# Optimization experiments

Hardware: AMD Instinct MI355X
Metric: run time of the kernel (lower is better)

## Reference

```python
import jax, jax.numpy as jnp
import numpy as np

B, J, L = 32, 16, 4096
MU_P = 0.15
MASK_ID = 103
VOCAB = 30522


def setup_inputs() -> dict:
    key = jax.random.key(0)
    k1, k2, k3 = jax.random.split(key, 3)
    input_ids = jax.random.randint(k1, (B, J, L), 0, VOCAB, dtype=jnp.int64 if jax.config.jax_enable_x64 else jnp.int32)
    # first half: nonnegative per-token weights; second half: shared-token ids (unused by the math)
    my_attention_mask = jax.random.uniform(k2, (B, J, 2 * L), dtype=jnp.float32)
    # uniform noise for Gumbel keys (weighted sampling w/o replacement)
    u = jax.random.uniform(k3, (B, J, L), dtype=jnp.float32, minval=1e-6, maxval=1.0)
    return {"input_ids": input_ids, "my_attention_mask": my_attention_mask, "u": u}


def reference(input_ids, my_attention_mask, u):
    # Split the mask: first half holds sampling weights (second half is unused).
    Lh = my_attention_mask.shape[-1] // 2
    w = my_attention_mask[..., :Lh]                       # [B, J, L]
    nz = w > 0                                            # valid positions
    cnt = nz.sum(axis=-1)                                 # [B, J] number of nonzero weights
    num_to_mask = jnp.floor(MU_P * cnt.astype(w.dtype)).astype(jnp.int32)  # int(mu_p * len)

    # Gumbel-key trick == weighted permutation without replacement over nonzero positions.
    g = -jnp.log(-jnp.log(u))
    scores = jnp.where(nz, jnp.log(jnp.maximum(w, 1e-30)) + g, -jnp.inf)
    # rank of each position in descending-score order
    rank = jnp.argsort(jnp.argsort(-scores, axis=-1), axis=-1)
    sel = (rank < num_to_mask[..., None]) & nz            # [B, J, L] positions to mask

    out_mask = sel.astype(w.dtype)
    out_ids = jnp.where(sel, jnp.asarray(MASK_ID, dtype=input_ids.dtype), input_ids)
    return out_ids, out_mask, -out_mask
```

## Files before the change

### kernel.cpp

```cpp
#include <hip/hip_runtime.h>

#define L_LEN 4096
#define NT 1024
#define ROWS 512
#define SLOP 96u
#define BCAP 256
#define NW (NT / 64)

__global__ __launch_bounds__(NT, 8) void AttentionEssentialReinforce_51238959841470_kernel(
    const int* __restrict__ ids,
    const float* __restrict__ amask,
    const float* __restrict__ uin,
    float* __restrict__ out,
    int n_per)
{
    __shared__ unsigned int hist[4096];
    __shared__ unsigned int h2[256];
    __shared__ unsigned int s_cntw[NW], s_orw[NW], s_nhiw[NW], s_wtot[NW];
    __shared__ unsigned long long bkey[BCAP];
    __shared__ int bidx[BCAP];
    __shared__ unsigned int s_remk, s_prefix, s_bn;

    const int row = blockIdx.x;
    const int tid = threadIdx.x;
    const int lane = tid & 63, wid = tid >> 6;
    const float* wrow = amask + (size_t)row * (2 * L_LEN);
    const float* urow = uin + (size_t)row * L_LEN;

    float4 a0 = reinterpret_cast<const float4*>(wrow)[tid];
    float4 b0 = reinterpret_cast<const float4*>(urow)[tid];
    unsigned odd = ((const unsigned*)ids)[2 * tid + 1];

    #pragma unroll
    for (int b = 0; b < 4096 / NT; ++b) hist[tid + b * NT] = 0u;
    if (tid < 256) h2[tid] = 0u;
    if (tid == 0) s_bn = 0u;

    float wv[4], uv[4];
    wv[0]=a0.x; wv[1]=a0.y; wv[2]=a0.z; wv[3]=a0.w;
    uv[0]=b0.x; uv[1]=b0.y; uv[2]=b0.z; uv[3]=b0.w;

    unsigned key[4];
    unsigned localnz = 0;
    #pragma unroll
    for (int e = 0; e < 4; ++e) {
        key[e] = 0u;
        if (wv[e] > 0.0f) {
            float t = -__logf(uv[e]);
            float r = __fdividef(fmaxf(wv[e], 1e-30f), t);
            key[e] = __float_as_uint(r);
            localnz++;
        }
    }
    {
        unsigned long long bal = __ballot(odd != 0u);
        unsigned v = localnz;
        #pragma unroll
        for (int off = 32; off > 0; off >>= 1) v += __shfl_down(v, off, 64);
        if (lane == 0) { s_cntw[wid] = v; s_orw[wid] = (bal != 0ull) ? 1u : 0u; }
    }
    __syncthreads();

    unsigned cnt = 0, orr = 0;
    #pragma unroll
    for (int w2 = 0; w2 < NW; ++w2) { cnt += s_cntw[w2]; orr |= s_orw[w2]; }
    const bool is64 = (orr == 0u);
    const int k = (int)floorf(0.15f * (float)cnt);

    int ida[4];
    if (!is64) {
        int4 t0 = reinterpret_cast<const int4*>(ids + (size_t)row * L_LEN)[tid];
        ida[0]=t0.x; ida[1]=t0.y; ida[2]=t0.z; ida[3]=t0.w;
    } else {
        const longlong2* idr = reinterpret_cast<const longlong2*>(
            (const long long*)ids + (size_t)row * L_LEN);
        longlong2 a = idr[2 * tid], b = idr[2 * tid + 1];
        ida[0]=(int)a.x; ida[1]=(int)a.y; ida[2]=(int)b.x; ida[3]=(int)b.y;
    }

    unsigned lo_thr = 0xFFFFFFFFu, hi_thr = 0xFFFFFFFFu;
    int need = 0;
    unsigned bn = 0;

    if (k > 0) {
        #pragma unroll
        for (int e = 0; e < 4; ++e) atomicAdd(&hist[key[e] >> 20], 1u);
        __syncthreads();
        {
            int b0i = 4095 - 4 * tid;
            unsigned c[4], lsum = 0;
            #pragma unroll
            for (int m = 0; m < 4; ++m) { c[m] = hist[b0i - m]; lsum += c[m]; }
            unsigned scan = lsum;
            #pragma unroll
            for (int off = 1; off < 64; off <<= 1) {
                unsigned o = __shfl_up(scan, (unsigned)off, 64);
                if (lane >= off) scan += o;
            }
            if (lane == 63) s_wtot[wid] = scan;
            __syncthreads();
            unsigned woff = 0;
            #pragma unroll
            for (int w2 = 0; w2 < NW; ++w2) woff += (w2 < wid) ? s_wtot[w2] : 0u;
            unsigned run = woff + (scan - lsum);
            unsigned remk = (unsigned)k;
            #pragma unroll
            for (int m = 0; m < 4; ++m) {
                if (run < remk && run + c[m] >= remk) {
                    s_prefix = (unsigned)(b0i - m);
                    s_remk = remk - run;
                }
                run += c[m];
            }
        }
        __syncthreads();
        unsigned prefix12 = s_prefix;
        unsigned remk = s_remk;

        #pragma unroll
        for (int e = 0; e < 4; ++e)
            if ((key[e] >> 20) == prefix12)
                atomicAdd(&h2[(key[e] >> 12) & 0xFFu], 1u);
        __syncthreads();
        if (tid < 64) {
            unsigned c[4], lsum = 0;
            #pragma unroll
            for (int m = 0; m < 4; ++m) { c[m] = h2[255 - 4 * tid - m]; lsum += c[m]; }
            unsigned scan = lsum;
            #pragma unroll
            for (int off = 1; off < 64; off <<= 1) {
                unsigned o = __shfl_up(scan, (unsigned)off, 64);
                if (tid >= off) scan += o;
            }
            unsigned run = scan - lsum;
            #pragma unroll
            for (int m = 0; m < 4; ++m) {
                if (run < remk && run + c[m] >= remk) {
                    s_prefix = (prefix12 << 8) | (unsigned)(255 - 4 * tid - m);
                }
                run += c[m];
            }
        }
        __syncthreads();
        const unsigned T20 = s_prefix;
        const unsigned B_lo = T20 << 12, B_hi = (T20 << 12) | 0xFFFu;

        lo_thr = (B_lo > SLOP) ? B_lo - SLOP : 1u;
        hi_thr = B_hi + SLOP;
        unsigned nhi = 0;
        #pragma unroll
        for (int e = 0; e < 4; ++e) {
            if (key[e] > hi_thr) {
                nhi++;
            } else if (key[e] >= lo_thr) {
                unsigned pos = atomicAdd(&s_bn, 1u);
                if (pos < BCAP) {
                    double t = -log((double)uv[e]);
                    double r = (double)fmaxf(wv[e], 1e-30f) / t;
                    bkey[pos] = (unsigned long long)__double_as_longlong(r);
                    bidx[pos] = 4 * tid + e;
                }
            }
        }
        {
            unsigned nv = nhi;
            #pragma unroll
            for (int off = 32; off > 0; off >>= 1) nv += __shfl_down(nv, off, 64);
            if (lane == 0) s_nhiw[wid] = nv;
        }
        __syncthreads();
        unsigned nhi_tot = 0;
        #pragma unroll
        for (int w2 = 0; w2 < NW; ++w2) nhi_tot += s_nhiw[w2];
        need = k - (int)nhi_tot;
        bn = s_bn; if (bn > BCAP) bn = BCAP;
    }

    const size_t obase = (size_t)row * L_LEN;
    float* o0 = out + obase;
    float* o1 = out + (size_t)n_per + obase;
    float* o2 = out + 2 * (size_t)n_per + obase;

    float f0[4], f1[4], f2[4];
    #pragma unroll
    for (int e = 0; e < 4; ++e) {
        bool sel;
        if (key[e] > hi_thr) {
            sel = true;
        } else if (key[e] < lo_thr) {
            sel = false;
        } else {
            double t = -log((double)uv[e]);
            double r = (double)fmaxf(wv[e], 1e-30f) / t;
            unsigned long long myk = (unsigned long long)__double_as_longlong(r);
            int myi = 4 * tid + e;
            int rnk = 0;
            for (unsigned j = 0; j < bn; ++j)
                rnk += (bkey[j] > myk) || (bkey[j] == myk && bidx[j] < myi);
            sel = (rnk < need);
        }
        f0[e] = sel ? 103.0f : (float)ida[e];
        f1[e] = sel ? 1.0f : 0.0f;
        f2[e] = sel ? -1.0f : -0.0f;
    }
    reinterpret_cast<float4*>(o0)[tid] = make_float4(f0[0], f0[1], f0[2], f0[3]);
    reinterpret_cast<float4*>(o1)[tid] = make_float4(f1[0], f1[1], f1[2], f1[3]);
    reinterpret_cast<float4*>(o2)[tid] = make_float4(f2[0], f2[1], f2[2], f2[3]);
}

extern "C" void kernel_launch(void* const* d_in, const int* in_sizes, int n_in,
                              void* d_out, int out_size, void* d_ws, size_t ws_size,
                              hipStream_t stream) {
    const int*   ids   = (const int*)d_in[0];
    const float* amask = (const float*)d_in[1];
    const float* uin   = (const float*)d_in[2];
    float* out = (float*)d_out;

    const int n_per = ROWS * L_LEN;

    AttentionEssentialReinforce_51238959841470_kernel<<<dim3(ROWS), dim3(NT), 0, stream>>>(
        ids, amask, uin, out, n_per);
}
```

Measured before the change: 86.56 us.

## Process two rows per block to hoist loads and overlap memory latency

Each 1024-thread block now handles two rows instead of one. All weight and noise loads for both rows, and the ids for both rows, are issued up front. The per-row selection phase is duplicated through a macro, with separate histogram and candidate buffers for each row. The goal is to hide global load latency behind the first row's compute, but the grid shrinks to 256 blocks on a GPU with many CUs, LDS per block doubles, and the launch-bounds occupancy hint drops.

```diff
diff --git a/kernel.cpp b/kernel.cpp
--- a/kernel.cpp
+++ b/kernel.cpp
@@ -7,205 +7,237 @@
 #define BCAP 256
 #define NW (NT / 64)
 
-__global__ __launch_bounds__(NT, 8) void AttentionEssentialReinforce_51238959841470_kernel(
+
+#define ROW_PHASE(R, AV, BV, IDA)                                                        \
+{                                                                                        \
+    float wv[4], uv[4];                                                                  \
+    wv[0]=AV.x; wv[1]=AV.y; wv[2]=AV.z; wv[3]=AV.w;                                      \
+    uv[0]=BV.x; uv[1]=BV.y; uv[2]=BV.z; uv[3]=BV.w;                                      \
+    unsigned key[4];                                                                     \
+    unsigned localnz = 0;                                                                \
+    _Pragma("unroll")                                                                    \
+    for (int e = 0; e < 4; ++e) {                                                        \
+        key[e] = 0u;                                 \
+        if (wv[e] > 0.0f) {                                                              \
+            float t = -__logf(uv[e]);                                                    \
+            float r = __fdividef(fmaxf(wv[e], 1e-30f), t);                               \
+            key[e] = __float_as_uint(r);                                                 \
+            localnz++;                                                                   \
+        }                                                                                \
+    }                                                                                    \
+    {                                                                                    \
+        unsigned v = localnz;                                                            \
+        _Pragma("unroll")                                                                \
+        for (int off = 32; off > 0; off >>= 1) v += __shfl_down(v, off, 64);             \
+        if (R == 0) {                                                                    \
+            unsigned long long bal = __ballot(odd != 0u);                                \
+            if (lane == 0) { s_cntw[R][wid] = v; s_orw[wid] = (bal != 0ull) ? 1u : 0u; } \
+        } else {                                                                         \
+            if (lane == 0) s_cntw[R][wid] = v;                                           \
+        }                                                                                \
+    }                                                                                    \
+    __syncthreads();                                     \
+    unsigned cnt = 0;                                                                    \
+    _Pragma("unroll")                                                                    \
+    for (int w2 = 0; w2 < NW; ++w2) cnt += s_cntw[R][w2];                                \
+    const int k = (int)floorf(0.15f * (float)cnt);      \
+    if (R == 0) {                                                                        \
+        unsigned orr = 0;                                                                \
+        _Pragma("unroll")                                                                \
+        for (int w2 = 0; w2 < NW; ++w2) orr |= s_orw[w2];                                \
+        is64 = (orr == 0u);                                                              \
+                  \
+                                         \
+        if (!is64) {                                                                     \
+            int4 t0 = reinterpret_cast<const int4*>(ids + (size_t)row0 * L_LEN)[tid];    \
+            ida0[0]=t0.x; ida0[1]=t0.y; ida0[2]=t0.z; ida0[3]=t0.w;                      \
+            int4 t1 = reinterpret_cast<const int4*>(ids + (size_t)(row0+1) * L_LEN)[tid];\
+            ida1[0]=t1.x; ida1[1]=t1.y; ida1[2]=t1.z; ida1[3]=t1.w;                      \
+        } else {                                                                         \
+            const long long* idp = (const long long*)ids;                                \
+            const longlong2* i0 = reinterpret_cast<const longlong2*>(                    \
+                idp + (size_t)row0 * L_LEN);                                             \
+            longlong2 a = i0[2 * tid], b = i0[2 * tid + 1];                              \
+            ida0[0]=(int)a.x; ida0[1]=(int)a.y; ida0[2]=(int)b.x; ida0[3]=(int)b.y;      \
+            const longlong2* i1 = reinterpret_cast<const longlong2*>(                    \
+                idp + (size_t)(row0 + 1) * L_LEN);                                       \
+            longlong2 c = i1[2 * tid], d = i1[2 * tid + 1];                              \
+            ida1[0]=(int)c.x; ida1[1]=(int)c.y; ida1[2]=(int)d.x; ida1[3]=(int)d.y;      \
+        }                                                                                \
+    }                                                                                    \
+    unsigned lo_thr = 0xFFFFFFFFu, hi_thr = 0xFFFFFFFFu;          \
+    int need = 0;                                                                        \
+    unsigned bn = 0;                                                                     \
+    if (k > 0) {                                                                         \
+                  \
+        _Pragma("unroll")                                                                \
+        for (int e = 0; e < 4; ++e) atomicAdd(&hist[R][key[e] >> 20], 1u);               \
+        __syncthreads();                                                                 \
+        {                                                                                \
+            int b0i = 4095 - 4 * tid;                  \
+            unsigned c[4], lsum = 0;                                                     \
+            _Pragma("unroll")                                                            \
+            for (int m = 0; m < 4; ++m) { c[m] = hist[R][b0i - m]; lsum += c[m]; }       \
+            unsigned scan = lsum;                                                        \
+            _Pragma("unroll")                                                            \
+            for (int off = 1; off < 64; off <<= 1) {                                     \
+                unsigned o = __shfl_up(scan, (unsigned)off, 64);                         \
+                if (lane >= off) scan += o;                                              \
+            }                                                                            \
+            if (lane == 63) s_wtot[wid] = scan;                                          \
+            __syncthreads();                                                             \
+            unsigned woff = 0;                             \
+            _Pragma("unroll")                                                            \
+            for (int w2 = 0; w2 < NW; ++w2) woff += (w2 < wid) ? s_wtot[w2] : 0u;        \
+            unsigned run = woff + (scan - lsum);      \
+            unsigned remk = (unsigned)k;                                                 \
+            _Pragma("unroll")                                                            \
+            for (int m = 0; m < 4; ++m) {                                                \
+                if (run < remk && run + c[m] >= remk) {             \
+                    s_prefix = (unsigned)(b0i - m);                                      \
+                    s_remk = remk - run;                                                 \
+                }                                                                        \
+                run += c[m];                                                             \
+            }                                                                            \
+        }                                                                                \
+        __syncthreads();                                                                 \
+        unsigned prefix12 = s_prefix;                                                    \
+        unsigned remk = s_remk;                                                          \
+                    \
+        _Pragma("unroll")                                                                \
+        for (int e = 0; e < 4; ++e)                                                      \
+            if ((key[e] >> 20) == prefix12)                                              \
+                atomicAdd(&h2[R][(key[e] >> 12) & 0xFFu], 1u);                           \
+        __syncthreads();                                                                 \
+        if (tid < 64) {                                 \
+            unsigned c[4], lsum = 0;                                                     \
+            _Pragma("unroll")                                                            \
+            for (int m = 0; m < 4; ++m) { c[m] = h2[R][255 - 4 * tid - m]; lsum += c[m]; }\
+            unsigned scan = lsum;                                                        \
+            _Pragma("unroll")                                                            \
+            for (int off = 1; off < 64; off <<= 1) {                                     \
+                unsigned o = __shfl_up(scan, (unsigned)off, 64);                         \
+                if (tid >= off) scan += o;                                               \
+            }                                                                            \
+            unsigned run = scan - lsum;                                                  \
+            _Pragma("unroll")                                                            \
+            for (int m = 0; m < 4; ++m) {                                                \
+                if (run < remk && run + c[m] >= remk) {                                  \
+                    s_prefix = (prefix12 << 8) | (unsigned)(255 - 4 * tid - m);          \
+                }                                                                        \
+                run += c[m];                                                             \
+            }                                                                            \
+        }                                                                                \
+        __syncthreads();                                                                 \
+        const unsigned T20 = s_prefix;                     \
+        const unsigned B_lo = T20 << 12, B_hi = (T20 << 12) | 0xFFFu;                    \
+                      \
+                                        \
+        lo_thr = (B_lo > SLOP) ? B_lo - SLOP : 1u;      \
+        hi_thr = B_hi + SLOP;                      \
+        unsigned nhi = 0;                                                                \
+        _Pragma("unroll")                                                                \
+        for (int e = 0; e < 4; ++e) {                                                    \
+            if (key[e] > hi_thr) {                                                       \
+                nhi++;                                                                   \
+            } else if (key[e] >= lo_thr) {                                               \
+                unsigned pos = atomicAdd(&s_bn[R], 1u);                                  \
+                if (pos < BCAP) {                                                        \
+                    double t = -log((double)uv[e]);                                      \
+                    double r = (double)fmaxf(wv[e], 1e-30f) / t;    \
+                    bkey[R][pos] = (unsigned long long)__double_as_longlong(r);          \
+                    bidx[R][pos] = 4 * tid + e;                                          \
+                }                                                                        \
+            }                                                                            \
+        }                                                                                \
+        {                                                                                \
+            unsigned nv = nhi;                                                           \
+            _Pragma("unroll")                                                            \
+            for (int off = 32; off > 0; off >>= 1) nv += __shfl_down(nv, off, 64);       \
+            if (lane == 0) s_nhiw[wid] = nv;                                             \
+        }                                                                                \
+        __syncthreads();                                                                 \
+        unsigned nhi_tot = 0;                                                            \
+        _Pragma("unroll")                                                                \
+        for (int w2 = 0; w2 < NW; ++w2) nhi_tot += s_nhiw[w2];                           \
+        need = k - (int)nhi_tot;                   \
+        bn = s_bn[R]; if (bn > BCAP) bn = BCAP;                                          \
+    }                                                                                    \
+                             \
+    const size_t obase = (size_t)(row0 + R) * L_LEN;                                     \
+    float* o0 = out + obase;                                                             \
+    float* o1 = out + (size_t)n_per + obase;                                             \
+    float* o2 = out + 2 * (size_t)n_per + obase;                                         \
+    float f0[4], f1[4], f2[4];                                                           \
+    _Pragma("unroll")                                                                    \
+    for (int e = 0; e < 4; ++e) {                                                        \
+        bool sel;                                                                        \
+        if (key[e] > hi_thr) {                                                           \
+            sel = true;                                                                  \
+        } else if (key[e] < lo_thr) {                                                    \
+            sel = false;                                                                 \
+        } else {                                                                         \
+                     \
+            double t = -log((double)uv[e]);                                              \
+            double r = (double)fmaxf(wv[e], 1e-30f) / t;                                 \
+            unsigned long long myk = (unsigned long long)__double_as_longlong(r);        \
+            int myi = 4 * tid + e;                                                       \
+            int rnk = 0;                                                                 \
+            for (unsigned j = 0; j < bn; ++j)                                            \
+                rnk += (bkey[R][j] > myk) || (bkey[R][j] == myk && bidx[R][j] < myi);    \
+            sel = (rnk < need);                                                          \
+        }                                                                                \
+        f0[e] = sel ? 103.0f : (float)IDA[e];                                            \
+        f1[e] = sel ? 1.0f : 0.0f;                                                       \
+        f2[e] = sel ? -1.0f : -0.0f;                                                     \
+    }                                                                                    \
+    reinterpret_cast<float4*>(o0)[tid] = make_float4(f0[0], f0[1], f0[2], f0[3]);        \
+    reinterpret_cast<float4*>(o1)[tid] = make_float4(f1[0], f1[1], f1[2], f1[3]);        \
+    reinterpret_cast<float4*>(o2)[tid] = make_float4(f2[0], f2[1], f2[2], f2[3]);        \
+}
+
+__global__ __launch_bounds__(NT, 4) void AttentionEssentialReinforce_51238959841470_kernel(
     const int* __restrict__ ids,
     const float* __restrict__ amask,
     const float* __restrict__ uin,
     float* __restrict__ out,
     int n_per)
 {
-    __shared__ unsigned int hist[4096];
-    __shared__ unsigned int h2[256];
-    __shared__ unsigned int s_cntw[NW], s_orw[NW], s_nhiw[NW], s_wtot[NW];
-    __shared__ unsigned long long bkey[BCAP];
-    __shared__ int bidx[BCAP];
-    __shared__ unsigned int s_remk, s_prefix, s_bn;
-
-    const int row = blockIdx.x;
+    __shared__ unsigned int hist[2][4096];
+    __shared__ unsigned int h2[2][256];
+    __shared__ unsigned int s_cntw[2][NW], s_orw[NW], s_nhiw[NW], s_wtot[NW];
+    __shared__ unsigned long long bkey[2][BCAP];
+    __shared__ int bidx[2][BCAP];
+    __shared__ unsigned int s_remk, s_prefix, s_bn[2];
+
     const int tid = threadIdx.x;
     const int lane = tid & 63, wid = tid >> 6;
-    const float* wrow = amask + (size_t)row * (2 * L_LEN);
-    const float* urow = uin + (size_t)row * L_LEN;
-
-    float4 a0 = reinterpret_cast<const float4*>(wrow)[tid];
-    float4 b0 = reinterpret_cast<const float4*>(urow)[tid];
+    const int row0 = 2 * blockIdx.x;
+
+    const float* w0 = amask + (size_t)row0 * (2 * L_LEN);
+    const float* w1 = amask + (size_t)(row0 + 1) * (2 * L_LEN);
+    const float* u0 = uin + (size_t)row0 * L_LEN;
+    const float* u1 = uin + (size_t)(row0 + 1) * L_LEN;
+
+    float4 av0 = reinterpret_cast<const float4*>(w0)[tid];
+    float4 bv0 = reinterpret_cast<const float4*>(u0)[tid];
+    float4 av1 = reinterpret_cast<const float4*>(w1)[tid];
+    float4 bv1 = reinterpret_cast<const float4*>(u1)[tid];
     unsigned odd = ((const unsigned*)ids)[2 * tid + 1];
 
-    #pragma unroll
-    for (int b = 0; b < 4096 / NT; ++b) hist[tid + b * NT] = 0u;
-    if (tid < 256) h2[tid] = 0u;
-    if (tid == 0) s_bn = 0u;
-
-    float wv[4], uv[4];
-    wv[0]=a0.x; wv[1]=a0.y; wv[2]=a0.z; wv[3]=a0.w;
-    uv[0]=b0.x; uv[1]=b0.y; uv[2]=b0.z; uv[3]=b0.w;
-
-    unsigned key[4];
-    unsigned localnz = 0;
-    #pragma unroll
-    for (int e = 0; e < 4; ++e) {
-        key[e] = 0u;
-        if (wv[e] > 0.0f) {
-            float t = -__logf(uv[e]);
-            float r = __fdividef(fmaxf(wv[e], 1e-30f), t);
-            key[e] = __float_as_uint(r);
-            localnz++;
-        }
+    {
+        unsigned* hf = &hist[0][0];
+        #pragma unroll
+        for (int b = 0; b < 8192 / NT; ++b) hf[tid + b * NT] = 0u;
     }
-    {
-        unsigned long long bal = __ballot(odd != 0u);
-        unsigned v = localnz;
-        #pragma unroll
-        for (int off = 32; off > 0; off >>= 1) v += __shfl_down(v, off, 64);
-        if (lane == 0) { s_cntw[wid] = v; s_orw[wid] = (bal != 0ull) ? 1u : 0u; }
-    }
-    __syncthreads();
-
-    unsigned cnt = 0, orr = 0;
-    #pragma unroll
-    for (int w2 = 0; w2 < NW; ++w2) { cnt += s_cntw[w2]; orr |= s_orw[w2]; }
-    const bool is64 = (orr == 0u);
-    const int k = (int)floorf(0.15f * (float)cnt);
-
-    int ida[4];
-    if (!is64) {
-        int4 t0 = reinterpret_cast<const int4*>(ids + (size_t)row * L_LEN)[tid];
-        ida[0]=t0.x; ida[1]=t0.y; ida[2]=t0.z; ida[3]=t0.w;
-    } else {
-        const longlong2* idr = reinterpret_cast<const longlong2*>(
-            (const long long*)ids + (size_t)row * L_LEN);
-        longlong2 a = idr[2 * tid], b = idr[2 * tid + 1];
-        ida[0]=(int)a.x; ida[1]=(int)a.y; ida[2]=(int)b.x; ida[3]=(int)b.y;
-    }
-
-    unsigned lo_thr = 0xFFFFFFFFu, hi_thr = 0xFFFFFFFFu;
-    int need = 0;
-    unsigned bn = 0;
-
-    if (k > 0) {
-        #pragma unroll
-        for (int e = 0; e < 4; ++e) atomicAdd(&hist[key[e] >> 20], 1u);
-        __syncthreads();
-        {
-            int b0i = 4095 - 4 * tid;
-            unsigned c[4], lsum = 0;
-            #pragma unroll
-            for (int m = 0; m < 4; ++m) { c[m] = hist[b0i - m]; lsum += c[m]; }
-            unsigned scan = lsum;
-            #pragma unroll
-            for (int off = 1; off < 64; off <<= 1) {
-                unsigned o = __shfl_up(scan, (unsigned)off, 64);
-                if (lane >= off) scan += o;
-            }
-            if (lane == 63) s_wtot[wid] = scan;
-            __syncthreads();
-            unsigned woff = 0;
-            #pragma unroll
-            for (int w2 = 0; w2 < NW; ++w2) woff += (w2 < wid) ? s_wtot[w2] : 0u;
-            unsigned run = woff + (scan - lsum);
-            unsigned remk = (unsigned)k;
-            #pragma unroll
-            for (int m = 0; m < 4; ++m) {
-                if (run < remk && run + c[m] >= remk) {
-                    s_prefix = (unsigned)(b0i - m);
-                    s_remk = remk - run;
-                }
-                run += c[m];
-            }
-        }
-        __syncthreads();
-        unsigned prefix12 = s_prefix;
-        unsigned remk = s_remk;
-
-        #pragma unroll
-        for (int e = 0; e < 4; ++e)
-            if ((key[e] >> 20) == prefix12)
-                atomicAdd(&h2[(key[e] >> 12) & 0xFFu], 1u);
-        __syncthreads();
-        if (tid < 64) {
-            unsigned c[4], lsum = 0;
-            #pragma unroll
-            for (int m = 0; m < 4; ++m) { c[m] = h2[255 - 4 * tid - m]; lsum += c[m]; }
-            unsigned scan = lsum;
-            #pragma unroll
-            for (int off = 1; off < 64; off <<= 1) {
-                unsigned o = __shfl_up(scan, (unsigned)off, 64);
-                if (tid >= off) scan += o;
-            }
-            unsigned run = scan - lsum;
-            #pragma unroll
-            for (int m = 0; m < 4; ++m) {
-                if (run < remk && run + c[m] >= remk) {
-                    s_prefix = (prefix12 << 8) | (unsigned)(255 - 4 * tid - m);
-                }
-                run += c[m];
-            }
-        }
-        __syncthreads();
-        const unsigned T20 = s_prefix;
-        const unsigned B_lo = T20 << 12, B_hi = (T20 << 12) | 0xFFFu;
-
-        lo_thr = (B_lo > SLOP) ? B_lo - SLOP : 1u;
-        hi_thr = B_hi + SLOP;
-        unsigned nhi = 0;
-        #pragma unroll
-        for (int e = 0; e < 4; ++e) {
-            if (key[e] > hi_thr) {
-                nhi++;
-            } else if (key[e] >= lo_thr) {
-                unsigned pos = atomicAdd(&s_bn, 1u);
-                if (pos < BCAP) {
-                    double t = -log((double)uv[e]);
-                    double r = (double)fmaxf(wv[e], 1e-30f) / t;
-                    bkey[pos] = (unsigned long long)__double_as_longlong(r);
-                    bidx[pos] = 4 * tid + e;
-                }
-            }
-        }
-        {
-            unsigned nv = nhi;
-            #pragma unroll
-            for (int off = 32; off > 0; off >>= 1) nv += __shfl_down(nv, off, 64);
-            if (lane == 0) s_nhiw[wid] = nv;
-        }
-        __syncthreads();
-        unsigned nhi_tot = 0;
-        #pragma unroll
-        for (int w2 = 0; w2 < NW; ++w2) nhi_tot += s_nhiw[w2];
-        need = k - (int)nhi_tot;
-        bn = s_bn; if (bn > BCAP) bn = BCAP;
-    }
-
-    const size_t obase = (size_t)row * L_LEN;
-    float* o0 = out + obase;
-    float* o1 = out + (size_t)n_per + obase;
-    float* o2 = out + 2 * (size_t)n_per + obase;
-
-    float f0[4], f1[4], f2[4];
-    #pragma unroll
-    for (int e = 0; e < 4; ++e) {
-        bool sel;
-        if (key[e] > hi_thr) {
-            sel = true;
-        } else if (key[e] < lo_thr) {
-            sel = false;
-        } else {
-            double t = -log((double)uv[e]);
-            double r = (double)fmaxf(wv[e], 1e-30f) / t;
-            unsigned long long myk = (unsigned long long)__double_as_longlong(r);
-            int myi = 4 * tid + e;
-            int rnk = 0;
-            for (unsigned j = 0; j < bn; ++j)
-                rnk += (bkey[j] > myk) || (bkey[j] == myk && bidx[j] < myi);
-            sel = (rnk < need);
-        }
-        f0[e] = sel ? 103.0f : (float)ida[e];
-        f1[e] = sel ? 1.0f : 0.0f;
-        f2[e] = sel ? -1.0f : -0.0f;
-    }
-    reinterpret_cast<float4*>(o0)[tid] = make_float4(f0[0], f0[1], f0[2], f0[3]);
-    reinterpret_cast<float4*>(o1)[tid] = make_float4(f1[0], f1[1], f1[2], f1[3]);
-    reinterpret_cast<float4*>(o2)[tid] = make_float4(f2[0], f2[1], f2[2], f2[3]);
+    if (tid < 256) { h2[0][tid] = 0u; h2[1][tid] = 0u; }
+    if (tid == 0) { s_bn[0] = 0u; s_bn[1] = 0u; }
+
+    bool is64 = false;
+    int ida0[4], ida1[4];
+
+    ROW_PHASE(0, av0, bv0, ida0)
+    ROW_PHASE(1, av1, bv1, ida1)
 }
 
 extern "C" void kernel_launch(void* const* d_in, const int* in_sizes, int n_in,
@@ -218,6 +250,6 @@
 
     const int n_per = ROWS * L_LEN;
 
-    AttentionEssentialReinforce_51238959841470_kernel<<<dim3(ROWS), dim3(NT), 0, stream>>>(
+    AttentionEssentialReinforce_51238959841470_kernel<<<dim3(ROWS / 2), dim3(NT), 0, stream>>>(
         ids, amask, uin, out, n_per);
 }
```

Result: slower. 90.08 us (+4.1%).
